# Performance work log

Measured on AMD Instinct MI355X. Metric: run time of the kernel, lower is better.

## Reference

```python
import jax, jax.numpy as jnp
import numpy as np

B, W, KD, NC, D, NN, NH, AD, HOPS = 512, 4, 64, 32, 256, 16, 8, 32, 4
DH = D // NH
DFF = 4 * D
P = B * W + B
ROLE_WRITER, ROLE_QUERY = 0, 1


def setup_inputs() -> dict:
    key = jax.random.key(0)
    ks = iter(jax.random.split(key, 40))
    f = lambda shape, s=0.02: jax.random.normal(next(ks), shape, dtype=jnp.float32) * s
    inp = {
        'query_keys': jax.random.normal(next(ks), (B, KD), dtype=jnp.float32),
        'writer_keys': jax.random.normal(next(ks), (B, W, KD), dtype=jnp.float32),
        'key_proj_w': f((KD, D)), 'key_proj_b': jnp.zeros((D,), jnp.float32),
        'class_embed': f((NC, D)), 'role_embed': f((3, D)), 'start_node_embed': f((NN, D)),
        'input_ln_g': jnp.ones((D,), jnp.float32), 'input_ln_b': jnp.zeros((D,), jnp.float32),
        'ln1_g': jnp.ones((NN, D), jnp.float32), 'ln1_b': jnp.zeros((NN, D), jnp.float32),
        'wqkv': f((NN, D, 3 * D)), 'bqkv': jnp.zeros((NN, 3 * D), jnp.float32),
        'wo': f((NN, D, D)), 'bo': jnp.zeros((NN, D), jnp.float32),
        'ln2_g': jnp.ones((NN, D), jnp.float32), 'ln2_b': jnp.zeros((NN, D), jnp.float32),
        'w_fc1': f((NN, D, DFF)), 'b_fc1': jnp.zeros((NN, DFF), jnp.float32),
        'w_fc2': f((NN, DFF, D)), 'b_fc2': jnp.zeros((NN, D), jnp.float32),
        'delta_w': jnp.zeros((D, D), jnp.float32), 'delta_b': jnp.zeros((D,), jnp.float32),
        'dir_w': f((D, D)), 'dir_b': jnp.zeros((D,), jnp.float32),
        'mag_w': f((D, 1)), 'mag_b': jnp.full((1,), 2.5, jnp.float32),
        'out_w': f((D, NC)), 'out_b': jnp.zeros((NC,), jnp.float32),
        'address_table': jax.random.normal(next(ks), (NN, AD), dtype=jnp.float32),
        'query_start_nodes': jax.random.randint(next(ks), (B,), 0, NN),
        'writer_labels': jax.random.randint(next(ks), (B, W), 0, NC),
        'writer_start_nodes': jax.random.randint(next(ks), (B, W), 0, NN),
    }
    return inp


def _ln(x):
    m = jnp.mean(x, -1, keepdims=True)
    v = jnp.var(x, -1, keepdims=True)
    return (x - m) * jax.lax.rsqrt(v + 1e-5)


def _forward(query_keys, writer_keys, key_proj_w, key_proj_b, class_embed, role_embed,
             start_node_embed, input_ln_g, input_ln_b, ln1_g, ln1_b, wqkv, bqkv, wo, bo,
             ln2_g, ln2_b, w_fc1, b_fc1, w_fc2, b_fc2, delta_w, delta_b, dir_w, dir_b,
             mag_w, mag_b, out_w, out_b, address_table,
             query_start_nodes, writer_labels, writer_start_nodes):
    # ---- encode writers (encode_writers) ----
    fk = writer_keys.reshape(-1, KD)          # [B*W, KD]
    fl = writer_labels.reshape(-1)            # [B*W]
    fs = writer_start_nodes.reshape(-1)       # [B*W]
    learned_w = fk @ key_proj_w + key_proj_b + class_embed[fl] + start_node_embed[fs] + role_embed[ROLE_WRITER]
    sw = jnp.zeros_like(learned_w).at[:, :KD].set(fk)
    sw = sw.at[:, KD:KD + NC].set(jax.nn.one_hot(fl, NC, dtype=learned_w.dtype))
    enc_w = _ln(learned_w) * input_ln_g + input_ln_b + sw
    # ---- encode queries (encode_queries) ----
    learned_q = query_keys @ key_proj_w + key_proj_b + start_node_embed[query_start_nodes] + role_embed[ROLE_QUERY]
    sq = jnp.zeros_like(learned_q).at[:, :KD].set(query_keys)
    enc_q = _ln(learned_q) * input_ln_g + input_ln_b + sq

    h = jnp.concatenate([enc_w, enc_q], axis=0)          # [P, D]
    node = jnp.concatenate([fs, query_start_nodes], 0)   # [P] current compute node per packet

    inv_sqrt_dh = 1.0 / np.sqrt(DH).astype(np.float32)
    for _ in range(HOPS):
        oh = jax.nn.one_hot(node, NN, dtype=h.dtype)      # [P, NN] dispatch weights

        def pnl(x, Wn, bn):
            # per-node linear: gather-compute-scatter via MoE-style dense dispatch
            xe = jnp.einsum('pn,pd->npd', oh, x)          # [NN, P, din]
            ye = jnp.einsum('npd,ndf->npf', xe, Wn)       # [NN, P, dout]
            return jnp.einsum('npf,pn->pf', ye, oh) + oh @ bn

        # ComputeNodeCell: pre-LN attention among packets at the same node
        x = _ln(h) * (oh @ ln1_g) + oh @ ln1_b
        qkv = pnl(x, wqkv, bqkv)                          # [P, 3D]
        q, k, v = jnp.split(qkv, 3, axis=-1)
        q = q.reshape(P, NH, DH); k = k.reshape(P, NH, DH); v = v.reshape(P, NH, DH)
        scores = jnp.einsum('phd,qhd->hpq', q, k) * inv_sqrt_dh   # [NH, P, P]
        same = node[:, None] == node[None, :]
        scores = jnp.where(same[None], scores, -1e9)
        attn = jax.nn.softmax(scores, axis=-1)
        ao = jnp.einsum('hpq,qhd->phd', attn, v).reshape(P, D)
        h = h + pnl(ao, wo, bo)
        # MLP block
        x2 = _ln(h) * (oh @ ln2_g) + oh @ ln2_b
        h = h + pnl(jax.nn.gelu(pnl(x2, w_fc1, b_fc1)), w_fc2, b_fc2)
        # routing heads: pick next node from address table, apply gated delta
        direction = h @ dir_w + dir_b
        node = jnp.argmax(direction[:, :AD] @ address_table.T, axis=-1)
        h = h + (h @ delta_w + delta_b) * jax.nn.sigmoid(h @ mag_w + mag_b)

    return h @ out_w + out_b                              # [P, NC] per-packet logits


def reference(query_keys, writer_keys, key_proj_w, key_proj_b, class_embed, role_embed,
              start_node_embed, input_ln_g, input_ln_b, ln1_g, ln1_b, wqkv, bqkv, wo, bo,
              ln2_g, ln2_b, w_fc1, b_fc1, w_fc2, b_fc2, delta_w, delta_b, dir_w, dir_b,
              mag_w, mag_b, out_w, out_b, address_table,
              query_start_nodes, writer_labels, writer_start_nodes):
    return _forward(query_keys, writer_keys, key_proj_w, key_proj_b, class_embed, role_embed,
                    start_node_embed, input_ln_g, input_ln_b, ln1_g, ln1_b, wqkv, bqkv, wo, bo,
                    ln2_g, ln2_b, w_fc1, b_fc1, w_fc2, b_fc2, delta_w, delta_b, dir_w, dir_b,
                    mag_w, mag_b, out_w, out_b, address_table,
                    query_start_nodes, writer_labels, writer_start_nodes)
```

## Files before the change

kernel.cpp:

```cpp
#include <hip/hip_runtime.h>
#include <math.h>

#define B_    512
#define W_    4
#define KD_   64
#define NC_   32
#define D_    256
#define NN_   16
#define NH_   8
#define AD_   32
#define HOPS_ 4
#define DH_   32
#define DFF_  1024
#define P_    2560
#define BW_   2048
#define MAXT3_ 96
#define PS_   (P_ + 32)

#define INV_SQRT_DH 0.17677669529663687f

typedef __attribute__((ext_vector_type(8))) short short8v;
typedef __attribute__((ext_vector_type(4))) float f32x4;

__device__ __forceinline__ unsigned short bf16_rne(float f) {
  unsigned u = __float_as_uint(f);
  unsigned r = (u + 0x7fffu + ((u >> 16) & 1u)) >> 16;
  return (unsigned short)r;
}
__device__ __forceinline__ void split2(float v, unsigned short& h, unsigned short& l) {
  unsigned short hb = bf16_rne(v);
  float hf = __uint_as_float(((unsigned)hb) << 16);
  h = hb;
  l = bf16_rne(v - hf);
}

__device__ __forceinline__ float block_sum256(float v, float* red) {
#pragma unroll
  for (int off = 32; off > 0; off >>= 1) v += __shfl_xor(v, off, 64);
  int wid = threadIdx.x >> 6;
  if ((threadIdx.x & 63) == 0) red[wid] = v;
  __syncthreads();
  float s = red[0] + red[1] + red[2] + red[3];
  __syncthreads();
  return s;
}

__device__ __forceinline__ float gelu_tanh(float v) {
  float u = 0.7978845608028654f * (v + 0.044715f * v * v * v);
  return 0.5f * v * (1.0f + tanhf(u));
}

__global__ __launch_bounds__(256) void padzero_kernel(unsigned short* __restrict__ xh,
                                                      unsigned short* __restrict__ xl,
                                                      unsigned short* __restrict__ ffh,
                                                      unsigned short* __restrict__ ffl) {
  int t = threadIdx.x;
  for (int i = t; i < 32 * D_; i += 256) {
    xh[(size_t)P_ * D_ + i] = 0;
    xl[(size_t)P_ * D_ + i] = 0;
  }
  for (int i = t; i < 32 * DFF_; i += 256) {
    ffh[(size_t)P_ * DFF_ + i] = 0;
    ffl[(size_t)P_ * DFF_ + i] = 0;
  }
}

__global__ __launch_bounds__(256) void encode_kernel(
    const float* __restrict__ query_keys, const float* __restrict__ writer_keys,
    const float* __restrict__ kpw, const float* __restrict__ kpb,
    const float* __restrict__ ce, const float* __restrict__ re,
    const float* __restrict__ sne, const float* __restrict__ ilg,
    const float* __restrict__ ilb, const int* __restrict__ qsn,
    const int* __restrict__ wl, const int* __restrict__ wsn,
    float* __restrict__ h, int* __restrict__ node) {
  int p = blockIdx.x, t = threadIdx.x;
  __shared__ float fk[KD_];
  __shared__ float red[4];
  const float* key;
  int lab = -1, sn, role;
  if (p < BW_) { key = writer_keys + (size_t)p * KD_; lab = wl[p]; sn = wsn[p]; role = 0; }
  else { int b = p - BW_; key = query_keys + (size_t)b * KD_; sn = qsn[b]; role = 1; }
  if (t < KD_) fk[t] = key[t];
  __syncthreads();

  float acc = kpb[t] + sne[sn * D_ + t] + re[role * D_ + t];
  if (lab >= 0) acc += ce[lab * D_ + t];
#pragma unroll 8
  for (int i = 0; i < KD_; i++) acc += fk[i] * kpw[i * D_ + t];

  float mean = block_sum256(acc, red) * (1.0f / D_);
  float d = acc - mean;
  float var = block_sum256(d * d, red) * (1.0f / D_);
  float xn = d * (1.0f / sqrtf(var + 1e-5f));

  float sw = 0.0f;
  if (t < KD_) sw = fk[t];
  else if (lab >= 0 && t < KD_ + NC_) sw = (t - KD_ == lab) ? 1.0f : 0.0f;

  h[(size_t)p * D_ + t] = xn * ilg[t] + ilb[t] + sw;
  if (t == 0) node[p] = sn;
}

__global__ __launch_bounds__(256) void sort_kernel(const int* __restrict__ node,
                                                   int* __restrict__ order,
                                                   int* __restrict__ offs,
                                                   int* __restrict__ cnts,
                                                   int* __restrict__ tnode32,
                                                   int* __restrict__ tstart32,
                                                   int* __restrict__ tend32,
                                                   int* __restrict__ ntiles32) {
  __shared__ int c[NN_], o[NN_], cur[NN_];
  int t = threadIdx.x;
  if (t < NN_) c[t] = 0;
  __syncthreads();
  for (int p = t; p < P_; p += 256) atomicAdd(&c[node[p]], 1);
  __syncthreads();
  if (t == 0) {
    int s = 0;
    for (int n = 0; n < NN_; n++) { o[n] = s; cur[n] = s; s += c[n]; }
    int i32 = 0;
    for (int n = 0; n < NN_; n++) {
      int e = o[n] + c[n];
      for (int m0 = o[n]; m0 < e; m0 += 32) {
        tnode32[i32] = n; tstart32[i32] = m0; tend32[i32] = e; i32++;
      }
    }
    ntiles32[0] = i32;
  }
  __syncthreads();
  if (t < NN_) { cnts[t] = c[t]; offs[t] = o[t]; }
  for (int p = t; p < P_; p += 256) {
    int r = atomicAdd(&cur[node[p]], 1);
    order[r] = p;
  }
}

__global__ __launch_bounds__(256) void ln_affine(const float* __restrict__ h,
                                                 const float* __restrict__ g,
                                                 const float* __restrict__ b,
                                                 const int* __restrict__ node,
                                                 const int* __restrict__ order,
                                                 unsigned short* __restrict__ xh,
                                                 unsigned short* __restrict__ xl) {
  int sp = blockIdx.x * 4 + (threadIdx.x >> 6);
  int lane = threadIdx.x & 63;
  int p = order[sp];
  int n = node[p];
  float4 v = *(const float4*)&h[(size_t)p * D_ + lane * 4];
  float s = v.x + v.y + v.z + v.w;
#pragma unroll
  for (int off = 32; off > 0; off >>= 1) s += __shfl_xor(s, off, 64);
  float mean = s * (1.0f / D_);
  float4 d = make_float4(v.x - mean, v.y - mean, v.z - mean, v.w - mean);
  float vr = d.x * d.x + d.y * d.y + d.z * d.z + d.w * d.w;
#pragma unroll
  for (int off = 32; off > 0; off >>= 1) vr += __shfl_xor(vr, off, 64);
  float inv = 1.0f / sqrtf(vr * (1.0f / D_) + 1e-5f);
  float4 gg = *(const float4*)&g[n * D_ + lane * 4];
  float4 bb = *(const float4*)&b[n * D_ + lane * 4];
  float o[4];
  o[0] = d.x * inv * gg.x + bb.x;
  o[1] = d.y * inv * gg.y + bb.y;
  o[2] = d.z * inv * gg.z + bb.z;
  o[3] = d.w * inv * gg.w + bb.w;
  ushort4 oh, ol;
  split2(o[0], oh.x, ol.x);
  split2(o[1], oh.y, ol.y);
  split2(o[2], oh.z, ol.z);
  split2(o[3], oh.w, ol.w);
  *(ushort4*)&xh[(size_t)sp * D_ + lane * 4] = oh;
  *(ushort4*)&xl[(size_t)sp * D_ + lane * 4] = ol;
}

template <int K, int C>
__global__ __launch_bounds__(256) void wprep(const float* __restrict__ W,
                                             unsigned short* __restrict__ th,
                                             unsigned short* __restrict__ tl) {
  __shared__ float ld[32][33];
  int n = blockIdx.z;
  int k0 = blockIdx.x * 32, c0 = blockIdx.y * 32;
  int tx = threadIdx.x & 31, ty = threadIdx.x >> 5;
  const float* Wn = W + (size_t)n * K * C;
#pragma unroll
  for (int i = 0; i < 32; i += 8)
    ld[i + ty][tx] = Wn[(size_t)(k0 + i + ty) * C + c0 + tx];
  __syncthreads();
#pragma unroll
  for (int i = 0; i < 32; i += 8) {
    float v = ld[tx][i + ty];
    unsigned short hh, ll;
    split2(v, hh, ll);
    size_t off = ((size_t)n * C + c0 + i + ty) * K + k0 + tx;
    th[off] = hh;
    tl[off] = ll;
  }
}

template <int DIN, int DOUT, int ACT, int RESID, int SPLITOUT, int DENSE, int HSPLIT>
__global__ __launch_bounds__(512) void gmfma(
    const unsigned short* __restrict__ xh, const unsigned short* __restrict__ xl,
    const unsigned short* __restrict__ wth, const unsigned short* __restrict__ wtl,
    const float* __restrict__ bias, float* __restrict__ outf,
    unsigned short* __restrict__ outh, unsigned short* __restrict__ outl,
    unsigned short* __restrict__ houth, unsigned short* __restrict__ houtl,
    const int* __restrict__ order, const int* __restrict__ tnode,
    const int* __restrict__ tstart, const int* __restrict__ tend,
    const int* __restrict__ ntiles) {
  constexpr int NCH = DIN / 64;
  __shared__ unsigned short ws[2][2][64][64];

  int gx = gridDim.x;
  int bid = blockIdx.x;
  int ti = (bid & 7) * (gx >> 3) + (bid >> 3);
  int n, s0, rows;
  if (DENSE) {
    n = 0;
    s0 = ti * 32;
    rows = 32;
  } else {
    if (ti >= ntiles[0]) return;
    n = tnode[ti];
    s0 = tstart[ti];
    rows = tend[ti] - s0;
    if (rows <= 0) return;
    if (rows > 32) rows = 32;
  }

  int tid = threadIdx.x;
  int wv = tid >> 6;
  int rh = wv >> 2;
  int wq = wv & 3;
  int lane = tid & 63;
  int r16 = lane & 15;
  int kg = lane >> 4;
  int jb = blockIdx.y * 64;

  const unsigned short* wsrc[2];
  int sj[2], c0j[2];
#pragma unroll
  for (int jj = 0; jj < 2; jj++) {
    int j = wv * 2 + jj;
    int s = j >> 3;
    int c0 = (j & 7) * 8;
    int c = c0 + (lane >> 3);
    int e = (lane & 7) ^ (c & 7);
    wsrc[jj] = ((e & 4) ? wtl : wth) +
               ((size_t)(n * DOUT + jb + c)) * DIN + s * 32 + (e & 3) * 8;
    sj[jj] = s;
    c0j[jj] = c0;
  }
  auto stage = [&](int buf, int kbase) {
#pragma unroll
    for (int jj = 0; jj < 2; jj++) {
      __builtin_amdgcn_global_load_lds(
          (const __attribute__((address_space(1))) unsigned int*)(wsrc[jj] + kbase),
          (__attribute__((address_space(3))) unsigned int*)&ws[buf][sj[jj]][c0j[jj]][0],
          16, 0, 0);
    }
  };

  const unsigned short* pah = xh + (size_t)(s0 + rh * 16 + r16) * DIN + kg * 8;
  const unsigned short* pal = xl + (size_t)(s0 + rh * 16 + r16) * DIN + kg * 8;

  short8v ah[2], al[2], nh[2], nl[2];
  auto afetch = [&](int kbase, short8v (&h_)[2], short8v (&l_)[2]) {
#pragma unroll
    for (int s = 0; s < 2; s++) {
      h_[s] = *(const short8v*)(pah + kbase + s * 32);
      l_[s] = *(const short8v*)(pal + kbase + s * 32);
    }
  };

  f32x4 acc0 = {0.f, 0.f, 0.f, 0.f};
  f32x4 acc1 = acc0, acc2 = acc0;
  int lcol = wq * 16 + r16;
  int ghi_ = (kg ^ (r16 & 7)) * 8;
  int glo_ = ((4 + kg) ^ (r16 & 7)) * 8;

  stage(0, 0);
  afetch(0, ah, al);
  __syncthreads();

  for (int ch = 0; ch < NCH; ch++) {
    int cur = ch & 1;
    if (ch + 1 < NCH) {
      stage(cur ^ 1, (ch + 1) * 64);
      afetch((ch + 1) * 64, nh, nl);
    }
#pragma unroll
    for (int s = 0; s < 2; s++) {
      short8v bh = *(const short8v*)&ws[cur][s][lcol][ghi_];
      short8v bl = *(const short8v*)&ws[cur][s][lcol][glo_];
      acc0 = __builtin_amdgcn_mfma_f32_16x16x32_bf16(ah[s], bh, acc0, 0, 0, 0);
      acc1 = __builtin_amdgcn_mfma_f32_16x16x32_bf16(ah[s], bl, acc1, 0, 0, 0);
      acc2 = __builtin_amdgcn_mfma_f32_16x16x32_bf16(al[s], bh, acc2, 0, 0, 0);
    }
    __syncthreads();
    if (ch + 1 < NCH) {
#pragma unroll
      for (int s = 0; s < 2; s++) { ah[s] = nh[s]; al[s] = nl[s]; }
    }
  }

  int jcol = jb + wq * 16;
  float bv = bias[(size_t)n * DOUT + jcol + r16];
#pragma unroll
  for (int rg = 0; rg < 4; rg++) {
    int r = rh * 16 + kg * 4 + rg;
    if (r >= rows) continue;
    float v = acc0[rg] + acc1[rg] + acc2[rg] + bv;
    if (ACT) v = gelu_tanh(v);
    if (SPLITOUT) {
      size_t off = (size_t)(s0 + r) * DOUT + jcol + r16;
      unsigned short hh, ll;
      split2(v, hh, ll);
      outh[off] = hh;
      outl[off] = ll;
    } else if (RESID) {
      int pp = DENSE ? (s0 + r) : order[s0 + r];
      size_t oidx = (size_t)pp * DOUT + jcol + r16;
      float nv = outf[oidx] + v;
      outf[oidx] = nv;
      if (HSPLIT) {
        unsigned short hh, ll;
        split2(nv, hh, ll);
        houth[oidx] = hh;
        houtl[oidx] = ll;
      }
    } else {
      outf[(size_t)(s0 + r) * DOUT + jcol + r16] = v;
    }
  }
}

#define ATS 36
__global__ __launch_bounds__(256) void attn_kernel(const float* __restrict__ qkv,
                                                   const int* __restrict__ node,
                                                   const int* __restrict__ order,
                                                   const int* __restrict__ offs,
                                                   const int* __restrict__ cnts,
                                                   unsigned short* __restrict__ aoh,
                                                   unsigned short* __restrict__ aol) {
  __shared__ float qs[32 * ATS];
  __shared__ float kts[2][32 * ATS];
  __shared__ float vs[2][32 * ATS];
  __shared__ float ps[32 * ATS];
  __shared__ int glo[32], ghi[32];

  int t = threadIdx.x;
  int r = t >> 3;
  int j4 = (t & 7) * 4;
  int r0 = blockIdx.x * 32;
  int hd = blockIdx.y;

  if (t < 32) {
    int n = node[order[r0 + t]];
    glo[t] = offs[n];
    ghi[t] = offs[n] + cnts[n];
  }
  __syncthreads();

  {
    const float* qp = &qkv[(size_t)(r0 + r) * 768 + hd * 32 + j4];
    float4 q4 = *(const float4*)qp;
    q4.x *= INV_SQRT_DH; q4.y *= INV_SQRT_DH; q4.z *= INV_SQRT_DH; q4.w *= INV_SQRT_DH;
    *(float4*)&qs[r * ATS + j4] = q4;
  }

  int lo = glo[0];
  int hi = ghi[31];
  int myglo = glo[r], myghi = ghi[r];
  int nt = (hi - lo + 31) >> 5;

  {
    int sj = lo + r;
    float4 k4 = {0.f, 0.f, 0.f, 0.f}, v4 = {0.f, 0.f, 0.f, 0.f};
    if (sj < hi) {
      const float* kp = &qkv[(size_t)sj * 768 + 256 + hd * 32 + j4];
      k4 = *(const float4*)kp;
      v4 = *(const float4*)(kp + 256);
    }
    kts[0][(j4 + 0) * ATS + r] = k4.x;
    kts[0][(j4 + 1) * ATS + r] = k4.y;
    kts[0][(j4 + 2) * ATS + r] = k4.z;
    kts[0][(j4 + 3) * ATS + r] = k4.w;
    *(float4*)&vs[0][r * ATS + j4] = v4;
  }
  __syncthreads();

  float4 o4 = {0.f, 0.f, 0.f, 0.f};
  float mrow = -1e30f, lrow = 0.f;

  for (int it = 0; it < nt; ++it) {
    int cb = it & 1;
    int kt = lo + it * 32;
    bool more = (it + 1 < nt);

    float4 kn = {0.f, 0.f, 0.f, 0.f}, vn = {0.f, 0.f, 0.f, 0.f};
    if (more) {
      int sj = kt + 32 + r;
      if (sj < hi) {
        const float* kp = &qkv[(size_t)sj * 768 + 256 + hd * 32 + j4];
        kn = *(const float4*)kp;
        vn = *(const float4*)(kp + 256);
      }
    }

    float s0 = 0.f, s1 = 0.f, s2 = 0.f, s3 = 0.f;
#pragma unroll 8
    for (int d = 0; d < 32; d++) {
      float qv = qs[r * ATS + d];
      float4 kv = *(const float4*)&kts[cb][d * ATS + j4];
      s0 += qv * kv.x; s1 += qv * kv.y; s2 += qv * kv.z; s3 += qv * kv.w;
    }
    int c0 = kt + j4;
    if (c0 + 0 < myglo || c0 + 0 >= myghi) s0 = -1e30f;
    if (c0 + 1 < myglo || c0 + 1 >= myghi) s1 = -1e30f;
    if (c0 + 2 < myglo || c0 + 2 >= myghi) s2 = -1e30f;
    if (c0 + 3 < myglo || c0 + 3 >= myghi) s3 = -1e30f;

    float mx = fmaxf(fmaxf(s0, s1), fmaxf(s2, s3));
#pragma unroll
    for (int off = 4; off > 0; off >>= 1) mx = fmaxf(mx, __shfl_xor(mx, off, 8));
    float mnew = fmaxf(mrow, mx);
    float alpha = __expf(mrow - mnew);
    float p0 = __expf(s0 - mnew), p1 = __expf(s1 - mnew);
    float p2 = __expf(s2 - mnew), p3 = __expf(s3 - mnew);
    float ls = p0 + p1 + p2 + p3;
#pragma unroll
    for (int off = 4; off > 0; off >>= 1) ls += __shfl_xor(ls, off, 8);
    lrow = lrow * alpha + ls;
    mrow = mnew;
    o4.x *= alpha; o4.y *= alpha; o4.z *= alpha; o4.w *= alpha;

    *(float4*)&ps[r * ATS + j4] = make_float4(p0, p1, p2, p3);
#pragma unroll 8
    for (int j = 0; j < 32; j++) {
      float pj = ps[r * ATS + j];
      float4 vv = *(const float4*)&vs[cb][j * ATS + j4];
      o4.x += pj * vv.x; o4.y += pj * vv.y; o4.z += pj * vv.z; o4.w += pj * vv.w;
    }

    if (more) {
      kts[cb ^ 1][(j4 + 0) * ATS + r] = kn.x;
      kts[cb ^ 1][(j4 + 1) * ATS + r] = kn.y;
      kts[cb ^ 1][(j4 + 2) * ATS + r] = kn.z;
      kts[cb ^ 1][(j4 + 3) * ATS + r] = kn.w;
      *(float4*)&vs[cb ^ 1][r * ATS + j4] = vn;
      __syncthreads();
    }
  }

  float inv = 1.f / lrow;
  o4.x *= inv; o4.y *= inv; o4.z *= inv; o4.w *= inv;
  ushort4 oh4, ol4;
  split2(o4.x, oh4.x, ol4.x);
  split2(o4.y, oh4.y, ol4.y);
  split2(o4.z, oh4.z, ol4.z);
  split2(o4.w, oh4.w, ol4.w);
  size_t off = (size_t)(r0 + r) * D_ + hd * 32 + j4;
  *(ushort4*)&aoh[off] = oh4;
  *(ushort4*)&aol[off] = ol4;
}

__global__ __launch_bounds__(256) void route_kernel(float* __restrict__ h,
                                                    const float* __restrict__ dir_w,
                                                    const float* __restrict__ dir_b,
                                                    const float* __restrict__ at,
                                                    const float* __restrict__ mag_w,
                                                    const float* __restrict__ mag_b,
                                                    const float* __restrict__ delta,
                                                    int* __restrict__ node) {
  int p = blockIdx.x, t = threadIdx.x;
  __shared__ float hs[D_];
  __shared__ float dpart[8][AD_];
  __shared__ float dirs[AD_];
  __shared__ float scs[NN_];
  __shared__ float red[4];
  float hv = h[(size_t)p * D_ + t];
  hs[t] = hv;
  __syncthreads();

  int j = t & 31, seg = t >> 5;
  float part = 0.0f;
#pragma unroll 8
  for (int i = 0; i < 32; i++) {
    int ii = seg * 32 + i;
    part += hs[ii] * dir_w[ii * D_ + j];
  }
  dpart[seg][j] = part;
  __syncthreads();
  if (t < AD_) {
    float s = dir_b[t];
#pragma unroll
    for (int g = 0; g < 8; g++) s += dpart[g][t];
    dirs[t] = s;
  }
  __syncthreads();
  if (t < NN_) {
    float s = 0.0f;
#pragma unroll
    for (int a = 0; a < AD_; a++) s += dirs[a] * at[t * AD_ + a];
    scs[t] = s;
  }
  __syncthreads();
  if (t == 0) {
    float best = scs[0];
    int arg = 0;
    for (int nn = 1; nn < NN_; nn++)
      if (scs[nn] > best) { best = scs[nn]; arg = nn; }
    node[p] = arg;
  }
  float mag = block_sum256(hv * mag_w[t], red) + mag_b[0];
  float sig = 1.0f / (1.0f + __expf(-mag));
  h[(size_t)p * D_ + t] = hv + delta[(size_t)p * D_ + t] * sig;
}

__global__ __launch_bounds__(256) void out_kernel(const float* __restrict__ h,
                                                  const float* __restrict__ ow,
                                                  const float* __restrict__ ob,
                                                  float* __restrict__ out) {
  int p = blockIdx.x, t = threadIdx.x;
  __shared__ float hs[D_];
  __shared__ float part[8][NC_];
  hs[t] = h[(size_t)p * D_ + t];
  __syncthreads();
  int j = t & 31, seg = t >> 5;
  float s = 0.0f;
#pragma unroll 8
  for (int i = 0; i < 32; i++) {
    int ii = seg * 32 + i;
    s += hs[ii] * ow[ii * NC_ + j];
  }
  part[seg][j] = s;
  __syncthreads();
  if (t < NC_) {
    float r = ob[t];
#pragma unroll
    for (int g = 0; g < 8; g++) r += part[g][t];
    out[(size_t)p * NC_ + t] = r;
  }
}

extern "C" void kernel_launch(void* const* d_in, const int* in_sizes, int n_in,
                              void* d_out, int out_size, void* d_ws, size_t ws_size,
                              hipStream_t stream) {
  (void)in_sizes; (void)n_in; (void)out_size; (void)ws_size;
  const float* query_keys       = (const float*)d_in[0];
  const float* writer_keys      = (const float*)d_in[1];
  const float* key_proj_w       = (const float*)d_in[2];
  const float* key_proj_b       = (const float*)d_in[3];
  const float* class_embed      = (const float*)d_in[4];
  const float* role_embed       = (const float*)d_in[5];
  const float* start_node_embed = (const float*)d_in[6];
  const float* input_ln_g       = (const float*)d_in[7];
  const float* input_ln_b       = (const float*)d_in[8];
  const float* ln1_g            = (const float*)d_in[9];
  const float* ln1_b            = (const float*)d_in[10];
  const float* wqkv             = (const float*)d_in[11];
  const float* bqkv             = (const float*)d_in[12];
  const float* wo               = (const float*)d_in[13];
  const float* bo               = (const float*)d_in[14];
  const float* ln2_g            = (const float*)d_in[15];
  const float* ln2_b            = (const float*)d_in[16];
  const float* w_fc1            = (const float*)d_in[17];
  const float* b_fc1            = (const float*)d_in[18];
  const float* w_fc2            = (const float*)d_in[19];
  const float* b_fc2            = (const float*)d_in[20];
  const float* delta_w          = (const float*)d_in[21];
  const float* delta_b          = (const float*)d_in[22];
  const float* dir_w            = (const float*)d_in[23];
  const float* dir_b            = (const float*)d_in[24];
  const float* mag_w            = (const float*)d_in[25];
  const float* mag_b            = (const float*)d_in[26];
  const float* out_w            = (const float*)d_in[27];
  const float* out_b            = (const float*)d_in[28];
  const float* address_table    = (const float*)d_in[29];
  const int* query_start_nodes  = (const int*)d_in[30];
  const int* writer_labels      = (const int*)d_in[31];
  const int* writer_start_nodes = (const int*)d_in[32];

  uintptr_t basep = (uintptr_t)d_ws;
  auto carve = [&](size_t bytes) {
    basep = (basep + 255) & ~(uintptr_t)255;
    void* r = (void*)basep;
    basep += bytes;
    return r;
  };
  float* h    = (float*)carve((size_t)P_ * D_ * 4);
  float* buf1 = (float*)carve((size_t)P_ * 768 * 4);
  unsigned short* xh  = (unsigned short*)carve((size_t)PS_ * D_ * 2);
  unsigned short* xl  = (unsigned short*)carve((size_t)PS_ * D_ * 2);
  unsigned short* ffh = (unsigned short*)carve((size_t)PS_ * DFF_ * 2);
  unsigned short* ffl = (unsigned short*)carve((size_t)PS_ * DFF_ * 2);
  unsigned short* hh  = (unsigned short*)carve((size_t)P_ * D_ * 2);
  unsigned short* hl  = (unsigned short*)carve((size_t)P_ * D_ * 2);
  unsigned short* wtqh = (unsigned short*)carve((size_t)NN_ * 768 * 256 * 2);
  unsigned short* wtql = (unsigned short*)carve((size_t)NN_ * 768 * 256 * 2);
  unsigned short* wt1h = (unsigned short*)carve((size_t)NN_ * 1024 * 256 * 2);
  unsigned short* wt1l = (unsigned short*)carve((size_t)NN_ * 1024 * 256 * 2);
  unsigned short* wt2h = (unsigned short*)carve((size_t)NN_ * 256 * 1024 * 2);
  unsigned short* wt2l = (unsigned short*)carve((size_t)NN_ * 256 * 1024 * 2);
  unsigned short* wtoh = (unsigned short*)carve((size_t)NN_ * 256 * 256 * 2);
  unsigned short* wtol = (unsigned short*)carve((size_t)NN_ * 256 * 256 * 2);
  unsigned short* dth  = (unsigned short*)carve((size_t)256 * 256 * 2);
  unsigned short* dtl  = (unsigned short*)carve((size_t)256 * 256 * 2);
  int* node   = (int*)carve(P_ * 4);
  int* order  = (int*)carve(P_ * 4);
  int* offs   = (int*)carve(NN_ * 4);
  int* cnts   = (int*)carve(NN_ * 4);
  int* tnode32  = (int*)carve(MAXT3_ * 4);
  int* tstart32 = (int*)carve(MAXT3_ * 4);
  int* tend32   = (int*)carve(MAXT3_ * 4);
  int* ntiles32 = (int*)carve(4);

  padzero_kernel<<<1, 256, 0, stream>>>(xh, xl, ffh, ffl);
  wprep<256, 768><<<dim3(8, 24, NN_), 256, 0, stream>>>(wqkv, wtqh, wtql);
  wprep<256, 1024><<<dim3(8, 32, NN_), 256, 0, stream>>>(w_fc1, wt1h, wt1l);
  wprep<1024, 256><<<dim3(32, 8, NN_), 256, 0, stream>>>(w_fc2, wt2h, wt2l);
  wprep<256, 256><<<dim3(8, 8, NN_), 256, 0, stream>>>(wo, wtoh, wtol);
  wprep<256, 256><<<dim3(8, 8, 1), 256, 0, stream>>>(delta_w, dth, dtl);

  encode_kernel<<<P_, 256, 0, stream>>>(query_keys, writer_keys, key_proj_w, key_proj_b,
                                        class_embed, role_embed, start_node_embed,
                                        input_ln_g, input_ln_b, query_start_nodes,
                                        writer_labels, writer_start_nodes, h, node);

  for (int hop = 0; hop < HOPS_; ++hop) {
    sort_kernel<<<1, 256, 0, stream>>>(node, order, offs, cnts,
                                       tnode32, tstart32, tend32, ntiles32);
    ln_affine<<<P_ / 4, 256, 0, stream>>>(h, ln1_g, ln1_b, node, order, xh, xl);
    gmfma<256, 768, 0, 0, 0, 0, 0><<<dim3(MAXT3_, 12), 512, 0, stream>>>(
        xh, xl, wtqh, wtql, bqkv, buf1, nullptr, nullptr, nullptr, nullptr,
        order, tnode32, tstart32, tend32, ntiles32);
    attn_kernel<<<dim3(P_ / 32, NH_), 256, 0, stream>>>(buf1, node, order, offs,
                                                        cnts, xh, xl);
    gmfma<256, 256, 0, 1, 0, 0, 0><<<dim3(MAXT3_, 4), 512, 0, stream>>>(
        xh, xl, wtoh, wtol, bo, h, nullptr, nullptr, nullptr, nullptr,
        order, tnode32, tstart32, tend32, ntiles32);
    ln_affine<<<P_ / 4, 256, 0, stream>>>(h, ln2_g, ln2_b, node, order, xh, xl);
    gmfma<256, 1024, 1, 0, 1, 0, 0><<<dim3(MAXT3_, 16), 512, 0, stream>>>(
        xh, xl, wt1h, wt1l, b_fc1, nullptr, ffh, ffl, nullptr, nullptr,
        order, tnode32, tstart32, tend32, ntiles32);
    gmfma<1024, 256, 0, 1, 0, 0, 1><<<dim3(MAXT3_, 4), 512, 0, stream>>>(
        ffh, ffl, wt2h, wt2l, b_fc2, h, nullptr, nullptr, hh, hl,
        order, tnode32, tstart32, tend32, ntiles32);
    gmfma<256, 256, 0, 0, 0, 1, 0><<<dim3(P_ / 32, 4), 512, 0, stream>>>(
        hh, hl, dth, dtl, delta_b, buf1, nullptr, nullptr, nullptr, nullptr,
        order, tnode32, tstart32, tend32, ntiles32);
    route_kernel<<<P_, 256, 0, stream>>>(h, dir_w, dir_b, address_table,
                                         mag_w, mag_b, buf1, node);
  }

  out_kernel<<<P_, 256, 0, stream>>>(h, out_w, out_b, (float*)d_out);
}
```

Before: 904.7 us.

## Restructure grouped MFMA GEMM to 4 waves with G row-groups per wave

The grouped GEMM kernel drops from 512 threads (8 waves, each on a 16-row half of a 32-row tile) to 256 threads (4 waves). Each wave now loops over G 16-row groups, so one staged weight tile is reused across 32 or 64 rows. The sort kernel now also emits a 64-row tile list, which the QKV, FC1 and FC2 GEMMs use, and the zero padding is widened to 64 rows. Activation fragments are now read straight from global memory inside the inner loop instead of being prefetched, so load latency may be exposed and register pressure rises with more accumulators.

Result: slower. 1.042 ms (+15.1%).

```diff
diff --git a/kernel.cpp b/kernel.cpp
--- a/kernel.cpp
+++ b/kernel.cpp
@@ -14,8 +14,9 @@
 #define DFF_  1024
 #define P_    2560
 #define BW_   2048
-#define MAXT3_ 96
-#define PS_   (P_ + 32)
+#define MAXT64_ 56
+#define MAXT32_ 96
+#define PS_   (P_ + 64)
 
 #define INV_SQRT_DH 0.17677669529663687f
 
@@ -55,11 +56,11 @@
                                                       unsigned short* __restrict__ ffh,
                                                       unsigned short* __restrict__ ffl) {
   int t = threadIdx.x;
-  for (int i = t; i < 32 * D_; i += 256) {
+  for (int i = t; i < 64 * D_; i += 256) {
     xh[(size_t)P_ * D_ + i] = 0;
     xl[(size_t)P_ * D_ + i] = 0;
   }
-  for (int i = t; i < 32 * DFF_; i += 256) {
+  for (int i = t; i < 64 * DFF_; i += 256) {
     ffh[(size_t)P_ * DFF_ + i] = 0;
     ffl[(size_t)P_ * DFF_ + i] = 0;
   }
@@ -105,6 +106,10 @@
                                                    int* __restrict__ order,
                                                    int* __restrict__ offs,
                                                    int* __restrict__ cnts,
+                                                   int* __restrict__ tnode64,
+                                                   int* __restrict__ tstart64,
+                                                   int* __restrict__ tend64,
+                                                   int* __restrict__ ntiles64,
                                                    int* __restrict__ tnode32,
                                                    int* __restrict__ tstart32,
                                                    int* __restrict__ tend32,
@@ -118,13 +123,17 @@
   if (t == 0) {
     int s = 0;
     for (int n = 0; n < NN_; n++) { o[n] = s; cur[n] = s; s += c[n]; }
-    int i32 = 0;
+    int i64 = 0, i32 = 0;
     for (int n = 0; n < NN_; n++) {
       int e = o[n] + c[n];
+      for (int m0 = o[n]; m0 < e; m0 += 64) {
+        tnode64[i64] = n; tstart64[i64] = m0; tend64[i64] = e; i64++;
+      }
       for (int m0 = o[n]; m0 < e; m0 += 32) {
         tnode32[i32] = n; tstart32[i32] = m0; tend32[i32] = e; i32++;
       }
     }
+    ntiles64[0] = i64;
     ntiles32[0] = i32;
   }
   __syncthreads();
@@ -196,8 +205,9 @@
   }
 }
 
-template <int DIN, int DOUT, int ACT, int RESID, int SPLITOUT, int DENSE, int HSPLIT>
-__global__ __launch_bounds__(512) void gmfma(
+template <int DIN, int DOUT, int G, int ACT, int RESID, int SPLITOUT, int DENSE,
+          int HSPLIT>
+__global__ __launch_bounds__(256) void gmfma(
     const unsigned short* __restrict__ xh, const unsigned short* __restrict__ xl,
     const unsigned short* __restrict__ wth, const unsigned short* __restrict__ wtl,
     const float* __restrict__ bias, float* __restrict__ outf,
@@ -207,6 +217,7 @@
     const int* __restrict__ tstart, const int* __restrict__ tend,
     const int* __restrict__ ntiles) {
   constexpr int NCH = DIN / 64;
+  constexpr int MT = G * 16;
   __shared__ unsigned short ws[2][2][64][64];
 
   int gx = gridDim.x;
@@ -215,31 +226,29 @@
   int n, s0, rows;
   if (DENSE) {
     n = 0;
-    s0 = ti * 32;
-    rows = 32;
+    s0 = ti * MT;
+    rows = MT;
   } else {
     if (ti >= ntiles[0]) return;
     n = tnode[ti];
     s0 = tstart[ti];
     rows = tend[ti] - s0;
     if (rows <= 0) return;
-    if (rows > 32) rows = 32;
+    if (rows > MT) rows = MT;
   }
 
   int tid = threadIdx.x;
   int wv = tid >> 6;
-  int rh = wv >> 2;
-  int wq = wv & 3;
   int lane = tid & 63;
   int r16 = lane & 15;
   int kg = lane >> 4;
   int jb = blockIdx.y * 64;
 
-  const unsigned short* wsrc[2];
-  int sj[2], c0j[2];
-#pragma unroll
-  for (int jj = 0; jj < 2; jj++) {
-    int j = wv * 2 + jj;
+  const unsigned short* wsrc[4];
+  int sj[4], c0j[4];
+#pragma unroll
+  for (int jj = 0; jj < 4; jj++) {
+    int j = wv * 4 + jj;
     int s = j >> 3;
     int c0 = (j & 7) * 8;
     int c = c0 + (lane >> 3);
@@ -251,7 +260,7 @@
   }
   auto stage = [&](int buf, int kbase) {
 #pragma unroll
-    for (int jj = 0; jj < 2; jj++) {
+    for (int jj = 0; jj < 4; jj++) {
       __builtin_amdgcn_global_load_lds(
           (const __attribute__((address_space(1))) unsigned int*)(wsrc[jj] + kbase),
           (__attribute__((address_space(3))) unsigned int*)&ws[buf][sj[jj]][c0j[jj]][0],
@@ -259,76 +268,74 @@
     }
   };
 
-  const unsigned short* pah = xh + (size_t)(s0 + rh * 16 + r16) * DIN + kg * 8;
-  const unsigned short* pal = xl + (size_t)(s0 + rh * 16 + r16) * DIN + kg * 8;
-
-  short8v ah[2], al[2], nh[2], nl[2];
-  auto afetch = [&](int kbase, short8v (&h_)[2], short8v (&l_)[2]) {
-#pragma unroll
-    for (int s = 0; s < 2; s++) {
-      h_[s] = *(const short8v*)(pah + kbase + s * 32);
-      l_[s] = *(const short8v*)(pal + kbase + s * 32);
-    }
-  };
-
-  f32x4 acc0 = {0.f, 0.f, 0.f, 0.f};
-  f32x4 acc1 = acc0, acc2 = acc0;
-  int lcol = wq * 16 + r16;
+  const unsigned short* pah = xh + (size_t)(s0 + r16) * DIN + kg * 8;
+  const unsigned short* pal = xl + (size_t)(s0 + r16) * DIN + kg * 8;
+
+  f32x4 acc0[G], acc1[G], acc2[G];
+#pragma unroll
+  for (int g = 0; g < G; g++) {
+    acc0[g] = f32x4{0.f, 0.f, 0.f, 0.f};
+    acc1[g] = f32x4{0.f, 0.f, 0.f, 0.f};
+    acc2[g] = f32x4{0.f, 0.f, 0.f, 0.f};
+  }
+  int lcol = wv * 16 + r16;
   int ghi_ = (kg ^ (r16 & 7)) * 8;
   int glo_ = ((4 + kg) ^ (r16 & 7)) * 8;
 
   stage(0, 0);
-  afetch(0, ah, al);
   __syncthreads();
 
   for (int ch = 0; ch < NCH; ch++) {
     int cur = ch & 1;
-    if (ch + 1 < NCH) {
-      stage(cur ^ 1, (ch + 1) * 64);
-      afetch((ch + 1) * 64, nh, nl);
-    }
-#pragma unroll
-    for (int s = 0; s < 2; s++) {
-      short8v bh = *(const short8v*)&ws[cur][s][lcol][ghi_];
-      short8v bl = *(const short8v*)&ws[cur][s][lcol][glo_];
-      acc0 = __builtin_amdgcn_mfma_f32_16x16x32_bf16(ah[s], bh, acc0, 0, 0, 0);
-      acc1 = __builtin_amdgcn_mfma_f32_16x16x32_bf16(ah[s], bl, acc1, 0, 0, 0);
-      acc2 = __builtin_amdgcn_mfma_f32_16x16x32_bf16(al[s], bh, acc2, 0, 0, 0);
+    if (ch + 1 < NCH) stage(cur ^ 1, (ch + 1) * 64);
+    int kb = ch * 64;
+#pragma unroll
+    for (int g = 0; g < G; g++) {
+      size_t ro = (size_t)g * 16 * DIN + kb;
+#pragma unroll
+      for (int s = 0; s < 2; s++) {
+        short8v ah = *(const short8v*)(pah + ro + s * 32);
+        short8v al = *(const short8v*)(pal + ro + s * 32);
+        short8v bh = *(const short8v*)&ws[cur][s][lcol][ghi_];
+        short8v bl = *(const short8v*)&ws[cur][s][lcol][glo_];
+        acc0[g] = __builtin_amdgcn_mfma_f32_16x16x32_bf16(ah, bh, acc0[g], 0, 0, 0);
+        acc1[g] = __builtin_amdgcn_mfma_f32_16x16x32_bf16(ah, bl, acc1[g], 0, 0, 0);
+        acc2[g] = __builtin_amdgcn_mfma_f32_16x16x32_bf16(al, bh, acc2[g], 0, 0, 0);
+      }
     }
     __syncthreads();
-    if (ch + 1 < NCH) {
-#pragma unroll
-      for (int s = 0; s < 2; s++) { ah[s] = nh[s]; al[s] = nl[s]; }
-    }
-  }
-
-  int jcol = jb + wq * 16;
+  }
+
+  int jcol = jb + wv * 16;
   float bv = bias[(size_t)n * DOUT + jcol + r16];
 #pragma unroll
-  for (int rg = 0; rg < 4; rg++) {
-    int r = rh * 16 + kg * 4 + rg;
-    if (r >= rows) continue;
-    float v = acc0[rg] + acc1[rg] + acc2[rg] + bv;
-    if (ACT) v = gelu_tanh(v);
-    if (SPLITOUT) {
-      size_t off = (size_t)(s0 + r) * DOUT + jcol + r16;
-      unsigned short hh, ll;
-      split2(v, hh, ll);
-      outh[off] = hh;
-      outl[off] = ll;
-    } else if (RESID) {
-      int pp = DENSE ? (s0 + r) : order[s0 + r];
-      size_t oidx = (size_t)pp * DOUT + jcol + r16;
-      float nv = outf[oidx] + v;
-      outf[oidx] = nv;
-      if (HSPLIT) {
+  for (int g = 0; g < G; g++) {
+#pragma unroll
+    for (int rg = 0; rg < 4; rg++) {
+      int r = g * 16 + kg * 4 + rg;
+      if (r >= rows) continue;
+      float v = acc0[g][rg] + acc1[g][rg] + acc2[g][rg] + bv;
+      if (ACT) v = gelu_tanh(v);
+      if (SPLITOUT) {
+        size_t off = (size_t)(s0 + r) * DOUT + jcol + r16;
         unsigned short hh, ll;
-        split2(nv, hh, ll);
-        houth[oidx] = hh;
-        houtl[oidx] = ll;
+        split2(v, hh, ll);
+        outh[off] = hh;
+        outl[off] = ll;
+      } else if (RESID) {
+        int pp = DENSE ? (s0 + r) : order[s0 + r];
+        size_t oidx = (size_t)pp * DOUT + jcol + r16;
+        float nv = outf[oidx] + v;
+        outf[oidx] = nv;
+        if (HSPLIT) {
+          unsigned short hh, ll;
+          split2(nv, hh, ll);
+          houth[oidx] = hh;
+          houtl[oidx] = ll;
+        }
+      } else {
+        outf[(size_t)(s0 + r) * DOUT + jcol + r16] = v;
       }
-    } else {
-      outf[(size_t)(s0 + r) * DOUT + jcol + r16] = v;
     }
   }
 }
@@ -609,9 +616,13 @@
   int* order  = (int*)carve(P_ * 4);
   int* offs   = (int*)carve(NN_ * 4);
   int* cnts   = (int*)carve(NN_ * 4);
-  int* tnode32  = (int*)carve(MAXT3_ * 4);
-  int* tstart32 = (int*)carve(MAXT3_ * 4);
-  int* tend32   = (int*)carve(MAXT3_ * 4);
+  int* tnode64  = (int*)carve(MAXT64_ * 4);
+  int* tstart64 = (int*)carve(MAXT64_ * 4);
+  int* tend64   = (int*)carve(MAXT64_ * 4);
+  int* ntiles64 = (int*)carve(4);
+  int* tnode32  = (int*)carve(MAXT32_ * 4);
+  int* tstart32 = (int*)carve(MAXT32_ * 4);
+  int* tend32   = (int*)carve(MAXT32_ * 4);
   int* ntiles32 = (int*)carve(4);
 
   padzero_kernel<<<1, 256, 0, stream>>>(xh, xl, ffh, ffl);
@@ -628,24 +639,25 @@
 
   for (int hop = 0; hop < HOPS_; ++hop) {
     sort_kernel<<<1, 256, 0, stream>>>(node, order, offs, cnts,
+                                       tnode64, tstart64, tend64, ntiles64,
                                        tnode32, tstart32, tend32, ntiles32);
     ln_affine<<<P_ / 4, 256, 0, stream>>>(h, ln1_g, ln1_b, node, order, xh, xl);
-    gmfma<256, 768, 0, 0, 0, 0, 0><<<dim3(MAXT3_, 12), 512, 0, stream>>>(
+    gmfma<256, 768, 4, 0, 0, 0, 0, 0><<<dim3(MAXT64_, 12), 256, 0, stream>>>(
         xh, xl, wtqh, wtql, bqkv, buf1, nullptr, nullptr, nullptr, nullptr,
-        order, tnode32, tstart32, tend32, ntiles32);
+        order, tnode64, tstart64, tend64, ntiles64);
     attn_kernel<<<dim3(P_ / 32, NH_), 256, 0, stream>>>(buf1, node, order, offs,
                                                         cnts, xh, xl);
-    gmfma<256, 256, 0, 1, 0, 0, 0><<<dim3(MAXT3_, 4), 512, 0, stream>>>(
+    gmfma<256, 256, 2, 0, 1, 0, 0, 0><<<dim3(MAXT32_, 4), 256, 0, stream>>>(
         xh, xl, wtoh, wtol, bo, h, nullptr, nullptr, nullptr, nullptr,
         order, tnode32, tstart32, tend32, ntiles32);
     ln_affine<<<P_ / 4, 256, 0, stream>>>(h, ln2_g, ln2_b, node, order, xh, xl);
-    gmfma<256, 1024, 1, 0, 1, 0, 0><<<dim3(MAXT3_, 16), 512, 0, stream>>>(
+    gmfma<256, 1024, 4, 1, 0, 1, 0, 0><<<dim3(MAXT64_, 16), 256, 0, stream>>>(
         xh, xl, wt1h, wt1l, b_fc1, nullptr, ffh, ffl, nullptr, nullptr,
-        order, tnode32, tstart32, tend32, ntiles32);
-    gmfma<1024, 256, 0, 1, 0, 0, 1><<<dim3(MAXT3_, 4), 512, 0, stream>>>(
+        order, tnode64, tstart64, tend64, ntiles64);
+    gmfma<1024, 256, 4, 0, 1, 0, 0, 1><<<dim3(MAXT64_, 4), 256, 0, stream>>>(
         ffh, ffl, wt2h, wt2l, b_fc2, h, nullptr, nullptr, hh, hl,
-        order, tnode32, tstart32, tend32, ntiles32);
-    gmfma<256, 256, 0, 0, 0, 1, 0><<<dim3(P_ / 32, 4), 512, 0, stream>>>(
+        order, tnode64, tstart64, tend64, ntiles64);
+    gmfma<256, 256, 2, 0, 0, 0, 1, 0><<<dim3(P_ / 32, 4), 256, 0, stream>>>(
         hh, hl, dth, dtl, delta_b, buf1, nullptr, nullptr, nullptr, nullptr,
         order, tnode32, tstart32, tend32, ntiles32);
     route_kernel<<<P_, 256, 0, stream>>>(h, dir_w, dir_b, address_table,
```
